# Optimization experiments

Hardware: AMD Instinct MI355X
Metric: run time of the kernel (lower is better)

The kernel has to match this reference:

```python
import jax, jax.numpy as jnp
import numpy as np

D = 768      # hidden_size
H = 12       # num_attention_heads
HD = D // H  # head_dim
F = 3072     # intermediate_size
B, S = 4, 2048
EPS = 1e-5


def _layer_norm(x, g, b):
    mu = jnp.mean(x, axis=-1, keepdims=True)
    var = jnp.mean(jnp.square(x - mu), axis=-1, keepdims=True)
    return (x - mu) * jax.lax.rsqrt(var + EPS) * g + b


def setup_inputs() -> dict:
    key = jax.random.key(0)
    ks = jax.random.split(key, 12)
    s_d = 1.0 / np.sqrt(D)
    s_f = 1.0 / np.sqrt(F)
    return {
        "x": jax.random.normal(ks[0], (B, S, D), jnp.float32),
        # per-head separate Q/K/V projections stacked along head axis [H, D, HD]
        "Wq": jax.random.normal(ks[1], (H, D, HD), jnp.float32) * s_d,
        "bq": jnp.zeros((H, HD), jnp.float32),
        "Wk": jax.random.normal(ks[2], (H, D, HD), jnp.float32) * s_d,
        "bk": jnp.zeros((H, HD), jnp.float32),
        "Wv": jax.random.normal(ks[3], (H, D, HD), jnp.float32) * s_d,
        "bv": jnp.zeros((H, HD), jnp.float32),
        "Wo": jax.random.normal(ks[4], (D, D), jnp.float32) * s_d,
        "bo": jnp.zeros((D,), jnp.float32),
        "W1": jax.random.normal(ks[5], (D, F), jnp.float32) * s_d,
        "b1": jnp.zeros((F,), jnp.float32),
        "W2": jax.random.normal(ks[6], (F, D), jnp.float32) * s_f,
        "b2": jnp.zeros((D,), jnp.float32),
        "g1": jnp.ones((D,), jnp.float32),
        "be1": jnp.zeros((D,), jnp.float32),
        "g2": jnp.ones((D,), jnp.float32),
        "be2": jnp.zeros((D,), jnp.float32),
    }


def reference(x, Wq, bq, Wk, bk, Wv, bv, Wo, bo, W1, b1, W2, b2, g1, be1, g2, be2):
    # NOTE: original module has NO residual connections; mask path is a no-op
    # (masked_fill is not in-place in the source), dropout is identity in eval.
    h = _layer_norm(x, g1, be1)
    # per-head projections: [B,H,S,HD]
    q = jnp.einsum('bsd,hde->bhse', h, Wq) + bq[None, :, None, :]
    k = jnp.einsum('bsd,hde->bhse', h, Wk) + bk[None, :, None, :]
    v = jnp.einsum('bsd,hde->bhse', h, Wv) + bv[None, :, None, :]
    scores = jnp.einsum('bhse,bhte->bhst', q, k) / jnp.sqrt(jnp.float32(HD))
    w = jax.nn.softmax(scores, axis=-1)          # [B,H,S,S]
    o = jnp.einsum('bhst,bhte->bhse', w, v)      # [B,H,S,HD]
    o = o.transpose(0, 2, 1, 3).reshape(B, S, D)  # concat heads along feature dim
    a = o @ Wo + bo
    h2 = _layer_norm(a, g2, be2)
    f = jax.nn.gelu(h2 @ W1 + b1, approximate=False)  # torch nn.GELU = exact erf
    return f @ W2 + b2
```

## Files before the change

### kernel.cpp

```cpp
#include <hip/hip_runtime.h>
#include <hip/hip_bf16.h>
#include <math.h>

typedef __hip_bfloat16 bf16;
typedef __attribute__((ext_vector_type(8))) short short8;
typedef __attribute__((ext_vector_type(4))) float f32x4;

#define D_  768
#define H_  12
#define HD_ 64
#define F_  3072
#define B_  4
#define S_  2048
#define BS_ (B_*S_)
#define SQK 1536
#define PSTR 72

__device__ __forceinline__ float b2f(bf16 x){ return __bfloat162float(x); }

union BU { bf16 b; unsigned short u; };
__device__ __forceinline__ bf16 f2b_fast(float x){
  BU t; t.u = (unsigned short)((__float_as_uint(x) + 0x8000u) >> 16); return t.b;
}
__device__ __forceinline__ unsigned pk2bf(float a, float b){
  return __builtin_amdgcn_perm(__float_as_uint(b) + 0x8000u,
                               __float_as_uint(a) + 0x8000u, 0x07060302u);
}

__device__ __forceinline__ f32x4 zero4(){ f32x4 z; z.x=0.f; z.y=0.f; z.z=0.f; z.w=0.f; return z; }

__device__ __forceinline__ f32x4 mfma16(uint4 a, uint4 b, f32x4 c){
  union U { uint4 u; short8 s; };
  U A, B; A.u = a; B.u = b;
  return __builtin_amdgcn_mfma_f32_16x16x32_bf16(A.s, B.s, c, 0, 0, 0);
}

typedef const __attribute__((address_space(1))) void gvoid;
typedef __attribute__((address_space(3))) void lvoid;
__device__ __forceinline__ void load_lds16(const void* g, void* l){
  __builtin_amdgcn_global_load_lds((gvoid*)g, (lvoid*)l, 16, 0, 0);
}

__device__ __forceinline__ float fast_gelu(float v){
  const float x = v * 0.70710678118654752f;
  const float ax = fabsf(x);
  const float t = __builtin_amdgcn_rcpf(fmaf(0.3275911f, ax, 1.0f));
  const float poly = t * fmaf(t, fmaf(t, fmaf(t, fmaf(t, 1.061405429f, -1.453152027f),
                                              1.421413741f), -0.284496736f), 0.254829592f);
  const float e = __builtin_amdgcn_exp2f(ax * ax * -1.4426950408889634f);
  const float erfax = 1.0f - poly * e;
  const float erfx = copysignf(erfax, x);
  return 0.5f * v * (1.0f + erfx);
}

__global__ __launch_bounds__(256)
void repack_t(const float* __restrict__ W, bf16* __restrict__ Wt, int K, int N)
{
  const int t = blockIdx.x * 256 + threadIdx.x;
  const int n = t % N;
  const int kg = t / N;
  const float* src = W + (size_t)kg * 8 * N + n;
  union { unsigned u32[4]; uint4 u; } pk;
#pragma unroll
  for (int j = 0; j < 4; ++j)
    pk.u32[j] = pk2bf(src[(size_t)(2 * j) * N], src[(size_t)(2 * j + 1) * N]);
  *(uint4*)(Wt + ((size_t)n * (K >> 3) + kg) * 8) = pk.u;
}

__global__ __launch_bounds__(256)
void repack_qkv_t(const float* __restrict__ Wq, const float* __restrict__ Wk,
                  const float* __restrict__ Wv, bf16* __restrict__ Wt)
{
  const int t = blockIdx.x * 256 + threadIdx.x;
  const int n = t % 2304;
  const int kg = t / 2304;
  const int sel = n / 768;
  const int nn = n - sel * 768;
  const int hh = nn >> 6;
  const int ee = nn & 63;
  const float* W = (sel == 0) ? Wq : (sel == 1) ? Wk : Wv;
  const float* src = W + ((size_t)hh * 768 + (size_t)kg * 8) * 64 + ee;
  union { unsigned u32[4]; uint4 u; } pk;
#pragma unroll
  for (int j = 0; j < 4; ++j)
    pk.u32[j] = pk2bf(src[(size_t)(2 * j) * 64], src[(size_t)(2 * j + 1) * 64]);
  *(uint4*)(Wt + ((size_t)n * 96 + kg) * 8) = pk.u;
}

__global__ __launch_bounds__(256)
void bias_qkv(const float* __restrict__ bq, const float* __restrict__ bk,
              const float* __restrict__ bv, float* __restrict__ out)
{
  const int t = blockIdx.x * 256 + threadIdx.x;
  out[t] = (t < 768) ? bq[t] : (t < 1536) ? bk[t - 768] : bv[t - 1536];
}

__global__ __launch_bounds__(256)
void ln_x_kernel(const float* __restrict__ X, const float* __restrict__ G,
                 const float* __restrict__ Bet, bf16* __restrict__ Y)
{
  const int t = threadIdx.x;
  const size_t row = blockIdx.x;
  const float* x = X + row * D_;
  float v0 = x[t], v1 = x[t + 256], v2 = x[t + 512];
  float s = v0 + v1 + v2;
#pragma unroll
  for (int d = 32; d >= 1; d >>= 1) s += __shfl_xor(s, d, 64);
  __shared__ float red[8];
  const int wv = t >> 6, ln = t & 63;
  if (ln == 0) red[wv] = s;
  __syncthreads();
  const float mu = (red[0] + red[1] + red[2] + red[3]) * (1.0f / 768.0f);
  const float d0 = v0 - mu, d1 = v1 - mu, d2 = v2 - mu;
  float sq = d0 * d0 + d1 * d1 + d2 * d2;
#pragma unroll
  for (int d = 32; d >= 1; d >>= 1) sq += __shfl_xor(sq, d, 64);
  if (ln == 0) red[4 + wv] = sq;
  __syncthreads();
  const float var = (red[4] + red[5] + red[6] + red[7]) * (1.0f / 768.0f);
  const float rs = rsqrtf(var + 1e-5f);
  bf16* y = Y + row * D_;
  y[t]       = f2b_fast(d0 * rs * G[t]       + Bet[t]);
  y[t + 256] = f2b_fast(d1 * rs * G[t + 256] + Bet[t + 256]);
  y[t + 512] = f2b_fast(d2 * rs * G[t + 512] + Bet[t + 512]);
}

__global__ __launch_bounds__(256)
void ln_h_kernel(const bf16* __restrict__ X, const float* __restrict__ G,
                 const float* __restrict__ Bet, bf16* __restrict__ Y)
{
  const int t = threadIdx.x;
  const size_t row = blockIdx.x;
  const bf16* x = X + row * D_;
  float v0 = b2f(x[t]), v1 = b2f(x[t + 256]), v2 = b2f(x[t + 512]);
  float s = v0 + v1 + v2;
#pragma unroll
  for (int d = 32; d >= 1; d >>= 1) s += __shfl_xor(s, d, 64);
  __shared__ float red[8];
  const int wv = t >> 6, ln = t & 63;
  if (ln == 0) red[wv] = s;
  __syncthreads();
  const float mu = (red[0] + red[1] + red[2] + red[3]) * (1.0f / 768.0f);
  const float d0 = v0 - mu, d1 = v1 - mu, d2 = v2 - mu;
  float sq = d0 * d0 + d1 * d1 + d2 * d2;
#pragma unroll
  for (int d = 32; d >= 1; d >>= 1) sq += __shfl_xor(sq, d, 64);
  if (ln == 0) red[4 + wv] = sq;
  __syncthreads();
  const float var = (red[4] + red[5] + red[6] + red[7]) * (1.0f / 768.0f);
  const float rs = rsqrtf(var + 1e-5f);
  bf16* y = Y + row * D_;
  y[t]       = f2b_fast(d0 * rs * G[t]       + Bet[t]);
  y[t + 256] = f2b_fast(d1 * rs * G[t + 256] + Bet[t + 256]);
  y[t + 512] = f2b_fast(d2 * rs * G[t + 512] + Bet[t + 512]);
}

__global__ __launch_bounds__(256)
void gemm_lds(const bf16* __restrict__ A, const bf16* __restrict__ Wt,
              const float* __restrict__ bias, bf16* __restrict__ C,
              bf16* __restrict__ Vp, float* __restrict__ Cf,
              int K, int N, int mode)
{
  __shared__ __align__(16) bf16 As[128 * 32];
  __shared__ __align__(16) bf16 Bs[128 * 32];

  const int tid = threadIdx.x;
  const int wave = tid >> 6, lane = tid & 63;
  const int l15 = lane & 15, qd = lane >> 4;
  const int wy = wave >> 1, wx = wave & 1;
  const size_t m0 = (size_t)blockIdx.y * 128;
  const int n0 = blockIdx.x * 128;

  const int r0 = tid >> 2, c0 = tid & 3;
  const bf16* Ag0 = A  + (m0 + r0) * (size_t)K + c0 * 8;
  const bf16* Ag1 = A  + (m0 + r0 + 64) * (size_t)K + c0 * 8;
  const bf16* Bg0 = Wt + (size_t)(n0 + r0) * K + c0 * 8;
  const bf16* Bg1 = Wt + (size_t)(n0 + r0 + 64) * K + c0 * 8;
  bf16* Al0 = As + (size_t)tid * 8;
  bf16* Al1 = As + (size_t)(tid + 256) * 8;
  bf16* Bl0 = Bs + (size_t)tid * 8;
  bf16* Bl1 = Bs + (size_t)(tid + 256) * 8;

  f32x4 acc[4][4];
#pragma unroll
  for (int i = 0; i < 4; ++i)
#pragma unroll
    for (int j = 0; j < 4; ++j) acc[i][j] = zero4();

  const int arow = wy * 64;
  const int brow = wx * 64;

  for (int k0 = 0; k0 < K; k0 += 32) {
    load_lds16(Ag0 + k0, Al0);
    load_lds16(Ag1 + k0, Al1);
    load_lds16(Bg0 + k0, Bl0);
    load_lds16(Bg1 + k0, Bl1);
    __syncthreads();
    uint4 af[4], bfr[4];
#pragma unroll
    for (int mt = 0; mt < 4; ++mt)
      af[mt] = *(const uint4*)(As + (size_t)(arow + mt * 16 + l15) * 32 + qd * 8);
#pragma unroll
    for (int nt = 0; nt < 4; ++nt)
      bfr[nt] = *(const uint4*)(Bs + (size_t)(brow + nt * 16 + l15) * 32 + qd * 8);
#pragma unroll
    for (int nt = 0; nt < 4; ++nt)
#pragma unroll
      for (int mt = 0; mt < 4; ++mt)
        acc[nt][mt] = mfma16(bfr[nt], af[mt], acc[nt][mt]);
    __syncthreads();
  }

  const size_t wm0 = m0 + arow;
  const int wn0 = n0 + brow;
#pragma unroll
  for (int nt = 0; nt < 4; ++nt) {
    const int nb = wn0 + nt * 16 + qd * 4;
    const f32x4 bs4 = *(const f32x4*)(bias + nb);
#pragma unroll
    for (int mt = 0; mt < 4; ++mt) {
      const size_t m = wm0 + mt * 16 + l15;
      float v[4];
#pragma unroll
      for (int r = 0; r < 4; ++r) v[r] = acc[nt][mt][r] + bs4[r];
      if (mode == 2) {
#pragma unroll
        for (int r = 0; r < 4; ++r) v[r] = fast_gelu(v[r]);
      }
      if (mode == 3) {
        f32x4 o; o.x = v[0]; o.y = v[1]; o.z = v[2]; o.w = v[3];
        *(f32x4*)(Cf + m * (size_t)N + nb) = o;
      } else if (mode == 0) {
        if (nb < SQK) {
          uint2 w; w.x = pk2bf(v[0], v[1]); w.y = pk2bf(v[2], v[3]);
          *(uint2*)(C + m * SQK + nb) = w;
        } else {
          const int bb = (int)(m >> 11);
          const int ss = (int)(m & 2047);
          const int hh = (nb - SQK) >> 6;
          const size_t vbase = (((size_t)bb * H_ + hh) * 256 + (ss >> 3)) * 512 + (ss & 7);
#pragma unroll
          for (int r = 0; r < 4; ++r)
            Vp[vbase + (size_t)((nb & 63) + r) * 8] = f2b_fast(v[r]);
        }
      } else {
        uint2 w; w.x = pk2bf(v[0], v[1]); w.y = pk2bf(v[2], v[3]);
        *(uint2*)(C + m * (size_t)N + nb) = w;
      }
    }
  }
}

__global__ __launch_bounds__(256, 3)
void attn_kernel(const bf16* __restrict__ QK, const bf16* __restrict__ Vp,
                 bf16* __restrict__ O)
{
  const int tid  = threadIdx.x;
  const int wave = tid >> 6;
  const int lane = tid & 63;
  const int l15 = lane & 15;
  const int qd  = lane >> 4;

  int bid = blockIdx.y * gridDim.x + blockIdx.x;
  bid = (bid & 7) * 96 + (bid >> 3);
  const int bh = bid >> 4;
  const int b  = bh / H_;
  const int h  = bh % H_;
  const int q0 = (bid & 15) * 128 + wave * 32;

  const bf16* Qb = QK + (size_t)b * S_ * SQK + h * HD_;
  const bf16* Kb = Qb + D_;
  const bf16* Vb = Vp + (size_t)bh * 256 * 512;

  __shared__ __align__(16) bf16 Ks[2][64 * 64];
  __shared__ __align__(16) bf16 Vs[2][8 * 512];
  __shared__ __align__(16) unsigned short Pl[4][32 * PSTR];
  unsigned short* Pw = &Pl[wave][0];

  const int srow = tid >> 3;
  const int sch  = (tid & 7) ^ (srow & 7);
  const bf16* Kst = Kb + (size_t)srow * SQK + sch * 8;
  const bf16* Vst = Vb + tid * 8;

  uint4 qf[2][2];
#pragma unroll
  for (int mt = 0; mt < 2; ++mt)
#pragma unroll
    for (int ks = 0; ks < 2; ++ks)
      qf[mt][ks] = *(const uint4*)(Qb + (size_t)(q0 + mt * 16 + l15) * SQK + ks * 32 + qd * 8);

  f32x4 o_[2][5];
#pragma unroll
  for (int mt = 0; mt < 2; ++mt)
#pragma unroll
    for (int dt = 0; dt < 5; ++dt) o_[mt][dt] = zero4();

  uint4 vones;
  { const unsigned v = (l15 == 0) ? 0x3F803F80u : 0u; vones.x = v; vones.y = v; vones.z = v; vones.w = v; }

  const float C1 = 1.4426950408889634f * 0.125f;
  const float C0 = -12.0f * 1.4426950408889634f;

  load_lds16(Kst,                      &Ks[0][tid * 8]);
  load_lds16(Kst + (size_t)32 * SQK,   &Ks[0][2048 + tid * 8]);
  load_lds16(Vst,                      &Vs[0][tid * 8]);
  load_lds16(Vst + 2048,               &Vs[0][2048 + tid * 8]);
  __syncthreads();

  for (int sk = 0; sk < S_; sk += 64) {
    const int cur = (sk >> 6) & 1;
    const bf16* Ksc = &Ks[cur][0];
    const bf16* Vsc = &Vs[cur][0];

    uint4 kf[4][2];
#pragma unroll
    for (int kt = 0; kt < 4; ++kt)
#pragma unroll
      for (int ks = 0; ks < 2; ++ks)
        kf[kt][ks] = *(const uint4*)(Ksc + (size_t)(kt * 16 + l15) * 64
                                         + ((ks * 4 + qd) ^ (l15 & 7)) * 8);
    uint4 vf[2][4];
#pragma unroll
    for (int ks = 0; ks < 2; ++ks)
#pragma unroll
      for (int dt = 0; dt < 4; ++dt)
        vf[ks][dt] = *(const uint4*)(Vsc + (ks * 4 + qd) * 512 + (dt * 16 + l15) * 8);

    if (sk + 64 < S_) {
      const int nxt = cur ^ 1;
      const bf16* Kn = Kst + (size_t)(sk + 64) * SQK;
      const bf16* Vn = Vst + (size_t)(sk + 64) * 64;
      load_lds16(Kn,                    &Ks[nxt][tid * 8]);
      load_lds16(Kn + (size_t)32 * SQK, &Ks[nxt][2048 + tid * 8]);
      load_lds16(Vn,                    &Vs[nxt][tid * 8]);
      load_lds16(Vn + 2048,             &Vs[nxt][2048 + tid * 8]);
    }

    f32x4 st[4][2];
#pragma unroll
    for (int kt = 0; kt < 4; ++kt)
#pragma unroll
      for (int mt = 0; mt < 2; ++mt) st[kt][mt] = zero4();
    __builtin_amdgcn_s_setprio(1);
#pragma unroll
    for (int ks = 0; ks < 2; ++ks)
#pragma unroll
      for (int kt = 0; kt < 4; ++kt)
#pragma unroll
        for (int mt = 0; mt < 2; ++mt)
          st[kt][mt] = mfma16(kf[kt][ks], qf[mt][ks], st[kt][mt]);
    __builtin_amdgcn_s_setprio(0);

#pragma unroll
    for (int mt = 0; mt < 2; ++mt) {
      unsigned short* prow = Pw + (mt * 16 + l15) * PSTR;
#pragma unroll
      for (int kt = 0; kt < 4; ++kt) {
        const float p0 = __builtin_amdgcn_exp2f(fmaf(st[kt][mt][0], C1, C0));
        const float p1 = __builtin_amdgcn_exp2f(fmaf(st[kt][mt][1], C1, C0));
        const float p2 = __builtin_amdgcn_exp2f(fmaf(st[kt][mt][2], C1, C0));
        const float p3 = __builtin_amdgcn_exp2f(fmaf(st[kt][mt][3], C1, C0));
        uint2 w; w.x = pk2bf(p0, p1); w.y = pk2bf(p2, p3);
        *(uint2*)(prow + kt * 16 + qd * 4) = w;
      }
    }

    uint4 pf[2][2];
#pragma unroll
    for (int mt = 0; mt < 2; ++mt)
#pragma unroll
      for (int ks = 0; ks < 2; ++ks)
        pf[mt][ks] = *(const uint4*)(Pw + (mt * 16 + l15) * PSTR + ks * 32 + qd * 8);

    __builtin_amdgcn_s_setprio(1);
#pragma unroll
    for (int ks = 0; ks < 2; ++ks)
#pragma unroll
      for (int mt = 0; mt < 2; ++mt) {
#pragma unroll
        for (int dt = 0; dt < 4; ++dt)
          o_[mt][dt] = mfma16(pf[mt][ks], vf[ks][dt], o_[mt][dt]);
        o_[mt][4] = mfma16(pf[mt][ks], vones, o_[mt][4]);
      }
    __builtin_amdgcn_s_setprio(0);

    __syncthreads();
  }

  const size_t tok0 = (size_t)b * S_ + q0;
#pragma unroll
  for (int mt = 0; mt < 2; ++mt) {
#pragma unroll
    for (int r = 0; r < 4; ++r) {
      const float lr = __shfl(o_[mt][4][r], (lane & 48), 64);
      const float inv = __builtin_amdgcn_rcpf(lr);
      const size_t row = tok0 + mt * 16 + qd * 4 + r;
#pragma unroll
      for (int dt = 0; dt < 4; ++dt)
        O[row * D_ + h * HD_ + dt * 16 + l15] = f2b_fast(o_[mt][dt][r] * inv);
    }
  }
}

extern "C" void kernel_launch(void* const* d_in, const int* in_sizes, int n_in,
                              void* d_out, int out_size, void* d_ws, size_t ws_size,
                              hipStream_t stream)
{
  const float* x   = (const float*)d_in[0];
  const float* Wq  = (const float*)d_in[1];
  const float* bq  = (const float*)d_in[2];
  const float* Wk  = (const float*)d_in[3];
  const float* bk  = (const float*)d_in[4];
  const float* Wv  = (const float*)d_in[5];
  const float* bv  = (const float*)d_in[6];
  const float* Wo  = (const float*)d_in[7];
  const float* bo  = (const float*)d_in[8];
  const float* W1  = (const float*)d_in[9];
  const float* b1  = (const float*)d_in[10];
  const float* W2  = (const float*)d_in[11];
  const float* b2  = (const float*)d_in[12];
  const float* g1  = (const float*)d_in[13];
  const float* be1 = (const float*)d_in[14];
  const float* g2  = (const float*)d_in[15];
  const float* be2 = (const float*)d_in[16];

  const bool full = ws_size >= (size_t)77079552;

  char* ws = (char*)d_ws;
  bf16* qk     = (bf16*)(ws + 0);
  bf16* vp     = (bf16*)(ws + 25165824);
  bf16* h1     = (bf16*)(ws + 37748736);
  bf16* obuf   = h1;
  bf16* abuf   = (bf16*)(ws + 0);
  bf16* h2     = (bf16*)(ws + (full ? 50331648u : 25165824u));
  bf16* fbuf   = (bf16*)(ws + 0);
  const size_t wb = full ? 62914560u : 50331648u;
  bf16* wqkv_p = (bf16*)(ws + wb);
  bf16* wo_p   = (bf16*)(ws + wb + 3538944u);
  bf16* w1_p   = (bf16*)(ws + wb + 4718592u);
  bf16* w2_p   = (bf16*)(ws + wb + 9437184u);
  float* bqkvf = (float*)(ws + wb + 14155776u);

  repack_qkv_t<<<dim3(864),  dim3(256), 0, stream>>>(Wq, Wk, Wv, wqkv_p);
  repack_t    <<<dim3(288),  dim3(256), 0, stream>>>(Wo, wo_p, 768, 768);
  repack_t    <<<dim3(1152), dim3(256), 0, stream>>>(W1, w1_p, 768, 3072);
  repack_t    <<<dim3(1152), dim3(256), 0, stream>>>(W2, w2_p, 3072, 768);
  bias_qkv    <<<dim3(9),    dim3(256), 0, stream>>>(bq, bk, bv, bqkvf);

  ln_x_kernel<<<dim3(BS_), dim3(256), 0, stream>>>(x, g1, be1, h1);
  gemm_lds<<<dim3(18, 64), dim3(256), 0, stream>>>(h1, wqkv_p, bqkvf, qk, vp, nullptr, 768, 2304, 0);
  attn_kernel<<<dim3(16, 48), dim3(256), 0, stream>>>(qk, vp, obuf);
  gemm_lds<<<dim3(6, 64),  dim3(256), 0, stream>>>(obuf, wo_p, bo, abuf, nullptr, nullptr, 768, 768, 1);
  ln_h_kernel<<<dim3(BS_), dim3(256), 0, stream>>>(abuf, g2, be2, h2);

  float* outp = (float*)d_out;
  if (full) {
    gemm_lds<<<dim3(24, 64), dim3(256), 0, stream>>>(h2, w1_p, b1, fbuf, nullptr, nullptr, 768, 3072, 2);
    gemm_lds<<<dim3(6, 64),  dim3(256), 0, stream>>>(fbuf, w2_p, b2, nullptr, nullptr, outp, 3072, 768, 3);
  } else {
    gemm_lds<<<dim3(24, 32), dim3(256), 0, stream>>>(h2, w1_p, b1, fbuf, nullptr, nullptr, 768, 3072, 2);
    gemm_lds<<<dim3(6, 32),  dim3(256), 0, stream>>>(fbuf, w2_p, b2, nullptr, nullptr, outp, 3072, 768, 3);
    gemm_lds<<<dim3(24, 32), dim3(256), 0, stream>>>(h2 + (size_t)4096 * D_, w1_p, b1, fbuf, nullptr, nullptr, 768, 3072, 2);
    gemm_lds<<<dim3(6, 32),  dim3(256), 0, stream>>>(fbuf, w2_p, b2, nullptr, nullptr, outp + (size_t)4096 * D_, 3072, 768, 3);
  }
}
```

Measured before the change: 461.1 us.

## Double-buffer GEMM LDS tiles, remap block ids across XCDs, split-K the W2 GEMM

```diff
diff --git a/kernel.cpp b/kernel.cpp
--- a/kernel.cpp
+++ b/kernel.cpp
@@ -96,6 +96,15 @@
 }
 
 __global__ __launch_bounds__(256)
+void prefill_bias(const float* __restrict__ b2, float* __restrict__ out)
+{
+  const int t = blockIdx.x * 256 + threadIdx.x;
+  const int col4 = t % 192;
+  const f32x4 bv = *(const f32x4*)(b2 + col4 * 4);
+  ((f32x4*)out)[t] = bv;
+}
+
+__global__ __launch_bounds__(256)
 void ln_x_kernel(const float* __restrict__ X, const float* __restrict__ G,
                  const float* __restrict__ Bet, bf16* __restrict__ Y)
 {
@@ -161,25 +170,33 @@
               bf16* __restrict__ Vp, float* __restrict__ Cf,
               int K, int N, int mode)
 {
-  __shared__ __align__(16) bf16 As[128 * 32];
-  __shared__ __align__(16) bf16 Bs[128 * 32];
+  __shared__ __align__(16) bf16 As[2][128 * 32];
+  __shared__ __align__(16) bf16 Bs[2][128 * 32];
 
   const int tid = threadIdx.x;
   const int wave = tid >> 6, lane = tid & 63;
   const int l15 = lane & 15, qd = lane >> 4;
   const int wy = wave >> 1, wx = wave & 1;
-  const size_t m0 = (size_t)blockIdx.y * 128;
-  const int n0 = blockIdx.x * 128;
+
+  int id = ((int)blockIdx.z * (int)gridDim.y + (int)blockIdx.y) * (int)gridDim.x
+           + (int)blockIdx.x;
+  const int chunk = ((int)gridDim.x * (int)gridDim.y * (int)gridDim.z) >> 3;
+  id = (id & 7) * chunk + (id >> 3);
+  const int bx = id % (int)gridDim.x;
+  const int t1 = id / (int)gridDim.x;
+  const int by = t1 % (int)gridDim.y;
+  const int bz = t1 / (int)gridDim.y;
+
+  const size_t m0 = (size_t)by * 128;
+  const int n0 = bx * 128;
+  const int Ksub = K / (int)gridDim.z;
+  const int koff = bz * Ksub;
 
   const int r0 = tid >> 2, c0 = tid & 3;
-  const bf16* Ag0 = A  + (m0 + r0) * (size_t)K + c0 * 8;
-  const bf16* Ag1 = A  + (m0 + r0 + 64) * (size_t)K + c0 * 8;
-  const bf16* Bg0 = Wt + (size_t)(n0 + r0) * K + c0 * 8;
-  const bf16* Bg1 = Wt + (size_t)(n0 + r0 + 64) * K + c0 * 8;
-  bf16* Al0 = As + (size_t)tid * 8;
-  bf16* Al1 = As + (size_t)(tid + 256) * 8;
-  bf16* Bl0 = Bs + (size_t)tid * 8;
-  bf16* Bl1 = Bs + (size_t)(tid + 256) * 8;
+  const bf16* Ag0 = A  + (m0 + r0) * (size_t)K + koff + c0 * 8;
+  const bf16* Ag1 = A  + (m0 + r0 + 64) * (size_t)K + koff + c0 * 8;
+  const bf16* Bg0 = Wt + (size_t)(n0 + r0) * K + koff + c0 * 8;
+  const bf16* Bg1 = Wt + (size_t)(n0 + r0 + 64) * K + koff + c0 * 8;
 
   f32x4 acc[4][4];
 #pragma unroll
@@ -190,19 +207,28 @@
   const int arow = wy * 64;
   const int brow = wx * 64;
 
-  for (int k0 = 0; k0 < K; k0 += 32) {
-    load_lds16(Ag0 + k0, Al0);
-    load_lds16(Ag1 + k0, Al1);
-    load_lds16(Bg0 + k0, Bl0);
-    load_lds16(Bg1 + k0, Bl1);
-    __syncthreads();
+  load_lds16(Ag0, &As[0][(size_t)tid * 8]);
+  load_lds16(Ag1, &As[0][(size_t)(tid + 256) * 8]);
+  load_lds16(Bg0, &Bs[0][(size_t)tid * 8]);
+  load_lds16(Bg1, &Bs[0][(size_t)(tid + 256) * 8]);
+  __syncthreads();
+
+  for (int k0 = 0; k0 < Ksub; k0 += 32) {
+    const int cur = (k0 >> 5) & 1;
+    if (k0 + 32 < Ksub) {
+      const int nxt = cur ^ 1;
+      load_lds16(Ag0 + k0 + 32, &As[nxt][(size_t)tid * 8]);
+      load_lds16(Ag1 + k0 + 32, &As[nxt][(size_t)(tid + 256) * 8]);
+      load_lds16(Bg0 + k0 + 32, &Bs[nxt][(size_t)tid * 8]);
+      load_lds16(Bg1 + k0 + 32, &Bs[nxt][(size_t)(tid + 256) * 8]);
+    }
     uint4 af[4], bfr[4];
 #pragma unroll
     for (int mt = 0; mt < 4; ++mt)
-      af[mt] = *(const uint4*)(As + (size_t)(arow + mt * 16 + l15) * 32 + qd * 8);
+      af[mt] = *(const uint4*)(&As[cur][0] + (size_t)(arow + mt * 16 + l15) * 32 + qd * 8);
 #pragma unroll
     for (int nt = 0; nt < 4; ++nt)
-      bfr[nt] = *(const uint4*)(Bs + (size_t)(brow + nt * 16 + l15) * 32 + qd * 8);
+      bfr[nt] = *(const uint4*)(&Bs[cur][0] + (size_t)(brow + nt * 16 + l15) * 32 + qd * 8);
 #pragma unroll
     for (int nt = 0; nt < 4; ++nt)
 #pragma unroll
@@ -216,7 +242,8 @@
 #pragma unroll
   for (int nt = 0; nt < 4; ++nt) {
     const int nb = wn0 + nt * 16 + qd * 4;
-    const f32x4 bs4 = *(const f32x4*)(bias + nb);
+    f32x4 bs4 = zero4();
+    if (mode != 3) bs4 = *(const f32x4*)(bias + nb);
 #pragma unroll
     for (int mt = 0; mt < 4; ++mt) {
       const size_t m = wm0 + mt * 16 + l15;
@@ -228,8 +255,9 @@
         for (int r = 0; r < 4; ++r) v[r] = fast_gelu(v[r]);
       }
       if (mode == 3) {
-        f32x4 o; o.x = v[0]; o.y = v[1]; o.z = v[2]; o.w = v[3];
-        *(f32x4*)(Cf + m * (size_t)N + nb) = o;
+#pragma unroll
+        for (int r = 0; r < 4; ++r)
+          atomicAdd(Cf + m * (size_t)N + nb + r, v[r]);
       } else if (mode == 0) {
         if (nb < SQK) {
           uint2 w; w.x = pk2bf(v[0], v[1]); w.y = pk2bf(v[2], v[3]);
@@ -441,11 +469,14 @@
   bf16* w2_p   = (bf16*)(ws + wb + 9437184u);
   float* bqkvf = (float*)(ws + wb + 14155776u);
 
+  float* outp = (float*)d_out;
+
   repack_qkv_t<<<dim3(864),  dim3(256), 0, stream>>>(Wq, Wk, Wv, wqkv_p);
   repack_t    <<<dim3(288),  dim3(256), 0, stream>>>(Wo, wo_p, 768, 768);
   repack_t    <<<dim3(1152), dim3(256), 0, stream>>>(W1, w1_p, 768, 3072);
   repack_t    <<<dim3(1152), dim3(256), 0, stream>>>(W2, w2_p, 3072, 768);
   bias_qkv    <<<dim3(9),    dim3(256), 0, stream>>>(bq, bk, bv, bqkvf);
+  prefill_bias<<<dim3(6144), dim3(256), 0, stream>>>(b2, outp);
 
   ln_x_kernel<<<dim3(BS_), dim3(256), 0, stream>>>(x, g1, be1, h1);
   gemm_lds<<<dim3(18, 64), dim3(256), 0, stream>>>(h1, wqkv_p, bqkvf, qk, vp, nullptr, 768, 2304, 0);
@@ -453,14 +484,13 @@
   gemm_lds<<<dim3(6, 64),  dim3(256), 0, stream>>>(obuf, wo_p, bo, abuf, nullptr, nullptr, 768, 768, 1);
   ln_h_kernel<<<dim3(BS_), dim3(256), 0, stream>>>(abuf, g2, be2, h2);
 
-  float* outp = (float*)d_out;
   if (full) {
     gemm_lds<<<dim3(24, 64), dim3(256), 0, stream>>>(h2, w1_p, b1, fbuf, nullptr, nullptr, 768, 3072, 2);
-    gemm_lds<<<dim3(6, 64),  dim3(256), 0, stream>>>(fbuf, w2_p, b2, nullptr, nullptr, outp, 3072, 768, 3);
+    gemm_lds<<<dim3(6, 64, 2), dim3(256), 0, stream>>>(fbuf, w2_p, nullptr, nullptr, nullptr, outp, 3072, 768, 3);
   } else {
     gemm_lds<<<dim3(24, 32), dim3(256), 0, stream>>>(h2, w1_p, b1, fbuf, nullptr, nullptr, 768, 3072, 2);
-    gemm_lds<<<dim3(6, 32),  dim3(256), 0, stream>>>(fbuf, w2_p, b2, nullptr, nullptr, outp, 3072, 768, 3);
+    gemm_lds<<<dim3(6, 32, 2), dim3(256), 0, stream>>>(fbuf, w2_p, nullptr, nullptr, nullptr, outp, 3072, 768, 3);
     gemm_lds<<<dim3(24, 32), dim3(256), 0, stream>>>(h2 + (size_t)4096 * D_, w1_p, b1, fbuf, nullptr, nullptr, 768, 3072, 2);
-    gemm_lds<<<dim3(6, 32),  dim3(256), 0, stream>>>(fbuf, w2_p, b2, nullptr, nullptr, outp + (size_t)4096 * D_, 3072, 768, 3);
+    gemm_lds<<<dim3(6, 32, 2), dim3(256), 0, stream>>>(fbuf, w2_p, nullptr, nullptr, nullptr, outp + (size_t)4096 * D_, 3072, 768, 3);
   }
 }
```

Result: slower. 546.6 us (+18.5%).
